# Performance work log

Measured on AMD Instinct MI355X. Metric: run time of the kernel, lower is better.

Reference implementation:

```python
import jax, jax.numpy as jnp
import numpy as np

B, N, C, H = 8, 8192, 256, 8  # batch, tokens, dim, heads


def setup_inputs() -> dict:
    key = jax.random.key(0)
    ks = jax.random.split(key, 12)
    p = lambda i, shape: jax.random.normal(ks[i], shape, jnp.float32) * 0.02
    return {
        "x0": jax.random.normal(ks[0], (B, N, C), jnp.float32),
        "x1": jax.random.normal(ks[1], (B, N, C), jnp.float32),
        # relation_judger MLP (shared by both directions)
        "fc1_w": p(2, (C, 2 * C)), "fc1_b": jnp.zeros((C,), jnp.float32),
        "fc2_w": p(3, (C, C)), "fc2_b": jnp.zeros((C,), jnp.float32),
        # cross_attn_0_to_1
        "in_w_01": p(4, (3 * C, C)), "in_b_01": jnp.zeros((3 * C,), jnp.float32),
        "out_w_01": p(5, (C, C)), "out_b_01": jnp.zeros((C,), jnp.float32),
        # cross_attn_1_to_0
        "in_w_10": p(6, (3 * C, C)), "in_b_10": jnp.zeros((3 * C,), jnp.float32),
        "out_w_10": p(7, (C, C)), "out_b_10": jnp.zeros((C,), jnp.float32),
        # noise embeddings (2 rows each)
        "k_noise": p(8, (2, C)), "v_noise": p(9, (2, C)),
    }


def _judge(a, b, fc1_w, fc1_b, fc2_w, fc2_b):
    # Mlp2(2C->C->C) + softmax over channels; torch GELU default = exact erf
    h = jax.nn.gelu(jnp.concatenate([a, b], axis=-1) @ fc1_w.T + fc1_b, approximate=False)
    return jax.nn.softmax(h @ fc2_w.T + fc2_b, axis=-1)


def _mha_kv2(q, k, v, Wi, bi, Wo, bo):
    # q: [B,N,C]; k,v: [B,N,2,C]. Each token attends over its own 2 kv slots
    # (matches torch MHA with batch_first=False, seq_q=1, seq_kv=2, batch=N).
    hd = C // H
    Q = (q @ Wi[:C].T + bi[:C]).reshape(B, N, H, hd)
    K = (k @ Wi[C:2 * C].T + bi[C:2 * C]).reshape(B, N, 2, H, hd)
    V = (v @ Wi[2 * C:].T + bi[2 * C:]).reshape(B, N, 2, H, hd)
    scores = jnp.einsum('bnhd,bnkhd->bnhk', Q, K) / jnp.sqrt(jnp.asarray(hd, q.dtype))
    attn = jax.nn.softmax(scores, axis=-1)  # [B,N,H,2]
    ctx = jnp.einsum('bnhk,bnkhd->bnhd', attn, V).reshape(B, N, C)
    return ctx @ Wo.T + bo


def reference(x0, x1, fc1_w, fc1_b, fc2_w, fc2_b,
              in_w_01, in_b_01, out_w_01, out_b_01,
              in_w_10, in_b_10, out_w_10, out_b_10,
              k_noise, v_noise):
    # noise expansion was under @torch.no_grad() -> detach noise weights
    kn = jax.lax.stop_gradient(k_noise)
    vn = jax.lax.stop_gradient(v_noise)

    rel01 = _judge(x0, x1, fc1_w, fc1_b, fc2_w, fc2_b)       # [B,N,C]
    k01 = jnp.stack([x0 + kn[0], x0 * rel01], axis=2)        # [B,N,2,C]
    v01 = jnp.stack([x0 + vn[0], x1], axis=2)
    out01 = _mha_kv2(x0, k01, v01, in_w_01, in_b_01, out_w_01, out_b_01)

    rel10 = _judge(x1, x0, fc1_w, fc1_b, fc2_w, fc2_b)
    k10 = jnp.stack([x1 + kn[1], x1 * rel10], axis=2)
    v10 = jnp.stack([x1 + vn[1], x0], axis=2)
    out10 = _mha_kv2(x1, k10, v10, in_w_10, in_b_10, out_w_10, out_b_10)

    return x0 + out01, x1 + out10
```

## Files before the change

### kernel.cpp

```cpp
#include <hip/hip_runtime.h>
#include <cstdint>
#include <cstddef>


typedef __attribute__((ext_vector_type(4))) float  f32x4;
typedef __attribute__((ext_vector_type(8))) short  short8;
typedef __attribute__((ext_vector_type(4))) float  float4_t;
typedef __attribute__((ext_vector_type(4))) unsigned short ushort4_t;

__device__ __forceinline__ float b2f(unsigned short u) {
  unsigned int x = ((unsigned int)u) << 16;
  return __builtin_bit_cast(float, x);
}
__device__ __forceinline__ unsigned short f2b(float f) {
  unsigned int u = __builtin_bit_cast(unsigned int, f);
  unsigned int r = (u + 0x7fffu + ((u >> 16) & 1u)) >> 16;
  return (unsigned short)r;
}

__device__ __forceinline__ void async16(const void* g, void* l) {
  __builtin_amdgcn_global_load_lds(
      (const __attribute__((address_space(1))) void*)g,
      (__attribute__((address_space(3))) void*)l, 16, 0, 0);
}

template <int EPI>
__global__ __launch_bounds__(256)
void gemm_bt(const unsigned short* __restrict__ A1,
             const unsigned short* __restrict__ A2,
             const unsigned short* __restrict__ W,
             int ldw, int koff2, int npairs,
             const float* __restrict__ bias,
             const float* __restrict__ res,
             void* __restrict__ outp, int ldo)
{
  __shared__ unsigned short Asm[128 * 32];
  __shared__ unsigned short Wsm[128 * 32];

  const int t = threadIdx.x;
  const size_t Arow0 = (size_t)blockIdx.x * 128;
  const int    Wrow0 = blockIdx.y * 128;

  const int l  = t & 63;
  const int wv = t >> 6;
  const int wr = (wv >> 1) * 64;
  const int wc = (wv & 1) * 64;
  const int lr = l & 15;
  const int kc = (l >> 4) * 8;

  const int srow = t >> 2;
  const int scol = (t & 3) * 8;

  f32x4 acc[4][4] = {};

  for (int p = 0; p < npairs; ++p) {
    const unsigned short* A = p ? A2 : A1;
    const int kb = p ? koff2 : 0;
    for (int kt = 0; kt < 8; ++kt) {
      const int k0 = kt * 32;
      __syncthreads();
      async16(&A[(Arow0 + srow) * 256 + (k0 + scol)],        &Asm[srow * 32 + scol]);
      async16(&A[(Arow0 + 64 + srow) * 256 + (k0 + scol)],   &Asm[(64 + srow) * 32 + scol]);
      async16(&W[(size_t)(Wrow0 + srow) * ldw + (kb + k0 + scol)],      &Wsm[srow * 32 + scol]);
      async16(&W[(size_t)(Wrow0 + 64 + srow) * ldw + (kb + k0 + scol)], &Wsm[(64 + srow) * 32 + scol]);
      __syncthreads();

      short8 af[4], bfr[4];
#pragma unroll
      for (int m = 0; m < 4; ++m)
        af[m] = *(const short8*)&Asm[(wr + m * 16 + lr) * 32 + kc];
#pragma unroll
      for (int n = 0; n < 4; ++n)
        bfr[n] = *(const short8*)&Wsm[(wc + n * 16 + lr) * 32 + kc];
#pragma unroll
      for (int m = 0; m < 4; ++m)
#pragma unroll
        for (int n = 0; n < 4; ++n)
          acc[m][n] = __builtin_amdgcn_mfma_f32_16x16x32_bf16(af[m], bfr[n], acc[m][n], 0, 0, 0);
    }
  }

  const int lq = l >> 4;
#pragma unroll
  for (int m = 0; m < 4; ++m) {
#pragma unroll
    for (int n = 0; n < 4; ++n) {
#pragma unroll
      for (int r = 0; r < 4; ++r) {
        size_t row = Arow0 + wr + m * 16 + lq * 4 + r;
        int col = Wrow0 + wc + n * 16 + lr;
        float v = acc[m][n][r] + bias[col];
        if (EPI == 1)
          v = 0.5f * v * (1.0f + erff(v * 0.70710678118654752f));
        if (EPI == 2)
          ((float*)outp)[row * (size_t)ldo + col] = v + res[row * 256 + col];
        else
          ((unsigned short*)outp)[row * (size_t)ldo + col] = f2b(v);
      }
    }
  }
}

__global__ __launch_bounds__(256)
void cvt_bf16(const float* __restrict__ src, unsigned short* __restrict__ dst, int n)
{
  int i = (blockIdx.x * 256 + threadIdx.x) * 4;
  if (i >= n) return;
  float4_t v = *(const float4_t*)(src + i);
  ushort4_t o;
  o[0] = f2b(v[0]); o[1] = f2b(v[1]); o[2] = f2b(v[2]); o[3] = f2b(v[3]);
  *(ushort4_t*)(dst + i) = o;
}

__global__ __launch_bounds__(256)
void softmax_rows(unsigned short* __restrict__ buf)
{
  int row = blockIdx.x * 4 + (threadIdx.x >> 6);
  int l = threadIdx.x & 63;
  unsigned short* p = buf + (size_t)row * 256;
  float v[4];
#pragma unroll
  for (int j = 0; j < 4; ++j) v[j] = b2f(p[l + 64 * j]);
  float mx = fmaxf(fmaxf(v[0], v[1]), fmaxf(v[2], v[3]));
#pragma unroll
  for (int off = 32; off > 0; off >>= 1) mx = fmaxf(mx, __shfl_xor(mx, off, 64));
  float s = 0.f;
#pragma unroll
  for (int j = 0; j < 4; ++j) { v[j] = expf(v[j] - mx); s += v[j]; }
#pragma unroll
  for (int off = 32; off > 0; off >>= 1) s += __shfl_xor(s, off, 64);
  float inv = 1.f / s;
#pragma unroll
  for (int j = 0; j < 4; ++j) p[l + 64 * j] = f2b(v[j] * inv);
}

__global__ __launch_bounds__(256)
void mul_bf16(const unsigned short* __restrict__ a,
              const unsigned short* __restrict__ b,
              unsigned short* __restrict__ o)
{
  size_t i = ((size_t)blockIdx.x * 256 + threadIdx.x) * 8;
  short8 va = *(const short8*)(a + i);
  short8 vb = *(const short8*)(b + i);
  short8 vo;
#pragma unroll
  for (int j = 0; j < 8; ++j)
    vo[j] = (short)f2b(b2f((unsigned short)va[j]) * b2f((unsigned short)vb[j]));
  *(short8*)(o + i) = vo;
}

__global__ __launch_bounds__(256)
void attn2(const unsigned short* __restrict__ qkv,
           const unsigned short* __restrict__ k1b,
           const unsigned short* __restrict__ v1b,
           unsigned short* __restrict__ ctx)
{
  int tid = blockIdx.x * 256 + threadIdx.x;
  int tok = tid >> 3;
  int h = tid & 7;
  const unsigned short* q   = qkv + (size_t)tok * 768 + h * 32;
  const unsigned short* k0p = q + 256;
  const unsigned short* v0p = q + 512;
  const unsigned short* k1p = k1b + (size_t)tok * 256 + h * 32;
  const unsigned short* v1p = v1b + (size_t)tok * 256 + h * 32;
  unsigned short* op = ctx + (size_t)tok * 256 + h * 32;

  float s0 = 0.f, s1 = 0.f;
#pragma unroll
  for (int c = 0; c < 4; ++c) {
    short8 q8 = *(const short8*)(q + c * 8);
    short8 a8 = *(const short8*)(k0p + c * 8);
    short8 b8 = *(const short8*)(k1p + c * 8);
#pragma unroll
    for (int j = 0; j < 8; ++j) {
      float qf = b2f((unsigned short)q8[j]);
      s0 += qf * b2f((unsigned short)a8[j]);
      s1 += qf * b2f((unsigned short)b8[j]);
    }
  }
  const float sc = 0.17677669529663687f;
  s0 *= sc; s1 *= sc;
  float mx = fmaxf(s0, s1);
  float e0 = expf(s0 - mx), e1 = expf(s1 - mx);
  float inv = 1.f / (e0 + e1);
  e0 *= inv; e1 *= inv;
#pragma unroll
  for (int c = 0; c < 4; ++c) {
    short8 a8 = *(const short8*)(v0p + c * 8);
    short8 b8 = *(const short8*)(v1p + c * 8);
    short8 o8;
#pragma unroll
    for (int j = 0; j < 8; ++j)
      o8[j] = (short)f2b(e0 * b2f((unsigned short)a8[j]) + e1 * b2f((unsigned short)b8[j]));
    *(short8*)(op + c * 8) = o8;
  }
}

__global__ __launch_bounds__(256)
void rowvec_k(const float* __restrict__ in_w, const float* __restrict__ in_b,
              const float* __restrict__ kn, const float* __restrict__ vn,
              int drow, float* __restrict__ rv)
{
  int j = blockIdx.x * 256 + threadIdx.x;
  float v = in_b[j];
  if (j >= 256) {
    const float* nz = (j < 512 ? kn : vn) + drow * 256;
    const float* wrow = in_w + (size_t)j * 256;
    float s = 0.f;
    for (int k = 0; k < 256; ++k) s += nz[k] * wrow[k];
    v += s;
  }
  rv[j] = v;
}

extern "C" void kernel_launch(void* const* d_in, const int* in_sizes, int n_in,
                              void* d_out, int out_size, void* d_ws, size_t ws_size,
                              hipStream_t stream)
{
  const float* x0     = (const float*)d_in[0];
  const float* x1     = (const float*)d_in[1];
  const float* fc1_w  = (const float*)d_in[2];
  const float* fc1_b  = (const float*)d_in[3];
  const float* fc2_w  = (const float*)d_in[4];
  const float* fc2_b  = (const float*)d_in[5];
  const float* in_w01 = (const float*)d_in[6];
  const float* in_b01 = (const float*)d_in[7];
  const float* out_w01= (const float*)d_in[8];
  const float* out_b01= (const float*)d_in[9];
  const float* in_w10 = (const float*)d_in[10];
  const float* in_b10 = (const float*)d_in[11];
  const float* out_w10= (const float*)d_in[12];
  const float* out_b10= (const float*)d_in[13];
  const float* kn     = (const float*)d_in[14];
  const float* vn     = (const float*)d_in[15];

  const size_t BN = (size_t)8 * 8192;
  const size_t NC = BN * 256;

  char* ws = (char*)d_ws;
  unsigned short* xb0   = (unsigned short*)ws; ws += NC * 2;
  unsigned short* xb1   = (unsigned short*)ws; ws += NC * 2;
  unsigned short* wfc1  = (unsigned short*)ws; ws += 131072 * 2;
  unsigned short* wfc2  = (unsigned short*)ws; ws += 65536 * 2;
  unsigned short* win01 = (unsigned short*)ws; ws += 196608 * 2;
  unsigned short* wout01= (unsigned short*)ws; ws += 65536 * 2;
  unsigned short* win10 = (unsigned short*)ws; ws += 196608 * 2;
  unsigned short* wout10= (unsigned short*)ws; ws += 65536 * 2;
  float* rv01 = (float*)ws; ws += 768 * 4;
  float* rv10 = (float*)ws; ws += 768 * 4;
  unsigned short* bufA = (unsigned short*)ws; ws += NC * 2;
  unsigned short* bufB = (unsigned short*)ws; ws += NC * 2;
  unsigned short* k1b  = (unsigned short*)ws; ws += NC * 2;
  unsigned short* v1b  = (unsigned short*)ws; ws += NC * 2;
  unsigned short* qkv  = (unsigned short*)ws; ws += BN * 768 * 2;

  size_t need = (size_t)(ws - (char*)d_ws);
  if (ws_size < need) return;

  dim3 blk(256);

  cvt_bf16<<<16384, blk, 0, stream>>>(x0, xb0, (int)NC);
  cvt_bf16<<<16384, blk, 0, stream>>>(x1, xb1, (int)NC);
  cvt_bf16<<<128, blk, 0, stream>>>(fc1_w, wfc1, 131072);
  cvt_bf16<<<64,  blk, 0, stream>>>(fc2_w, wfc2, 65536);
  cvt_bf16<<<192, blk, 0, stream>>>(in_w01, win01, 196608);
  cvt_bf16<<<64,  blk, 0, stream>>>(out_w01, wout01, 65536);
  cvt_bf16<<<192, blk, 0, stream>>>(in_w10, win10, 196608);
  cvt_bf16<<<64,  blk, 0, stream>>>(out_w10, wout10, 65536);
  rowvec_k<<<3, blk, 0, stream>>>(in_w01, in_b01, kn, vn, 0, rv01);
  rowvec_k<<<3, blk, 0, stream>>>(in_w10, in_b10, kn, vn, 1, rv10);

  for (int d = 0; d < 2; ++d) {
    const unsigned short* xa  = d ? xb1 : xb0;
    const unsigned short* xo  = d ? xb0 : xb1;
    const float* xaf  = d ? x1 : x0;
    const unsigned short* win  = d ? win10 : win01;
    const unsigned short* wout = d ? wout10 : wout01;
    const float* inb  = d ? in_b10 : in_b01;
    const float* outb = d ? out_b10 : out_b01;
    const float* rv   = d ? rv10 : rv01;
    float* outp = (float*)d_out + (size_t)d * NC;

    dim3 g2(512, 2), g6(512, 6);

    gemm_bt<1><<<g2, blk, 0, stream>>>(xa, xo, wfc1, 512, 256, 2,
                                       fc1_b, nullptr, bufA, 256);
    gemm_bt<0><<<g2, blk, 0, stream>>>(bufA, nullptr, wfc2, 256, 0, 1,
                                       fc2_b, nullptr, bufB, 256);
    softmax_rows<<<16384, blk, 0, stream>>>(bufB);
    mul_bf16<<<8192, blk, 0, stream>>>(xa, bufB, bufA);
    gemm_bt<0><<<g6, blk, 0, stream>>>(xa, nullptr, win, 256, 0, 1,
                                       rv, nullptr, qkv, 768);
    gemm_bt<0><<<g2, blk, 0, stream>>>(bufA, nullptr, win + 256 * 256, 256, 0, 1,
                                       inb + 256, nullptr, k1b, 256);
    gemm_bt<0><<<g2, blk, 0, stream>>>(xo, nullptr, win + 512 * 256, 256, 0, 1,
                                       inb + 512, nullptr, v1b, 256);
    attn2<<<2048, blk, 0, stream>>>(qkv, k1b, v1b, bufB);
    gemm_bt<2><<<g2, blk, 0, stream>>>(bufB, nullptr, wout, 256, 0, 1,
                                       outb, xaf, outp, 256);
  }
}
```

Measured before the change: 844.8 us.

## Batch both directions into merged GEMM launches with swizzled LDS and fused softmax-mul

Both attention directions are processed in single launches. One large GEMM kernel computes QKV, the cross V projection and fc1+GELU from a concatenated weight matrix, and later GEMMs cover both halves. The LDS layout is XOR-swizzled to cut bank conflicts, and workgroup IDs are remapped into chunks for cache locality. Softmax and the elementwise multiply are fused, and the conversion and prep kernels are merged. This cuts launch count and intermediate traffic, at the cost of more complex indexing and buffer aliasing (ctx reuses xb).

```diff
diff --git a/kernel.cpp b/kernel.cpp
--- a/kernel.cpp
+++ b/kernel.cpp
@@ -2,6 +2,10 @@
 #include <cstdint>
 #include <cstddef>
 
+
+#define BNv  65536
+#define TBNv 131072
+#define NCv  16777216ull
 
 typedef __attribute__((ext_vector_type(4))) float  f32x4;
 typedef __attribute__((ext_vector_type(8))) short  short8;
@@ -24,34 +28,25 @@
       (__attribute__((address_space(3))) void*)l, 16, 0, 0);
 }
 
-template <int EPI>
-__global__ __launch_bounds__(256)
-void gemm_bt(const unsigned short* __restrict__ A1,
-             const unsigned short* __restrict__ A2,
-             const unsigned short* __restrict__ W,
-             int ldw, int koff2, int npairs,
-             const float* __restrict__ bias,
-             const float* __restrict__ res,
-             void* __restrict__ outp, int ldo)
-{
-  __shared__ unsigned short Asm[128 * 32];
-  __shared__ unsigned short Wsm[128 * 32];
-
-  const int t = threadIdx.x;
-  const size_t Arow0 = (size_t)blockIdx.x * 128;
-  const int    Wrow0 = blockIdx.y * 128;
-
+__device__ __forceinline__ void mfma_loop(
+    const unsigned short* __restrict__ A1,
+    const unsigned short* __restrict__ A2,
+    const unsigned short* __restrict__ W,
+    int ldw, int koff2, int npairs,
+    size_t Arow0, int Wrow0,
+    unsigned short* Asm, unsigned short* Wsm,
+    f32x4 (&acc)[4][4], int t)
+{
   const int l  = t & 63;
   const int wv = t >> 6;
   const int wr = (wv >> 1) * 64;
   const int wc = (wv & 1) * 64;
   const int lr = l & 15;
-  const int kc = (l >> 4) * 8;
-
-  const int srow = t >> 2;
-  const int scol = (t & 3) * 8;
-
-  f32x4 acc[4][4] = {};
+  const int kcS = (((l >> 4) ^ ((lr >> 1) & 3)) * 8);
+
+  const int srow  = t >> 2;
+  const int scolS = (((t & 3) ^ ((t >> 3) & 3)) * 8);
+  const int ldst  = t * 8;
 
   for (int p = 0; p < npairs; ++p) {
     const unsigned short* A = p ? A2 : A1;
@@ -59,19 +54,19 @@
     for (int kt = 0; kt < 8; ++kt) {
       const int k0 = kt * 32;
       __syncthreads();
-      async16(&A[(Arow0 + srow) * 256 + (k0 + scol)],        &Asm[srow * 32 + scol]);
-      async16(&A[(Arow0 + 64 + srow) * 256 + (k0 + scol)],   &Asm[(64 + srow) * 32 + scol]);
-      async16(&W[(size_t)(Wrow0 + srow) * ldw + (kb + k0 + scol)],      &Wsm[srow * 32 + scol]);
-      async16(&W[(size_t)(Wrow0 + 64 + srow) * ldw + (kb + k0 + scol)], &Wsm[(64 + srow) * 32 + scol]);
+      async16(&A[(Arow0 + srow) * 256 + (size_t)(k0 + scolS)],        &Asm[ldst]);
+      async16(&A[(Arow0 + 64 + srow) * 256 + (size_t)(k0 + scolS)],   &Asm[64 * 32 + ldst]);
+      async16(&W[(size_t)(Wrow0 + srow) * ldw + (kb + k0 + scolS)],      &Wsm[ldst]);
+      async16(&W[(size_t)(Wrow0 + 64 + srow) * ldw + (kb + k0 + scolS)], &Wsm[64 * 32 + ldst]);
       __syncthreads();
 
       short8 af[4], bfr[4];
 #pragma unroll
       for (int m = 0; m < 4; ++m)
-        af[m] = *(const short8*)&Asm[(wr + m * 16 + lr) * 32 + kc];
+        af[m] = *(const short8*)&Asm[(wr + m * 16 + lr) * 32 + kcS];
 #pragma unroll
       for (int n = 0; n < 4; ++n)
-        bfr[n] = *(const short8*)&Wsm[(wc + n * 16 + lr) * 32 + kc];
+        bfr[n] = *(const short8*)&Wsm[(wc + n * 16 + lr) * 32 + kcS];
 #pragma unroll
       for (int m = 0; m < 4; ++m)
 #pragma unroll
@@ -79,31 +74,160 @@
           acc[m][n] = __builtin_amdgcn_mfma_f32_16x16x32_bf16(af[m], bfr[n], acc[m][n], 0, 0, 0);
     }
   }
-
-  const int lq = l >> 4;
+}
+
+template <int EPI>
+__device__ __forceinline__ void store_tile(
+    f32x4 (&acc)[4][4], int t,
+    const float* __restrict__ bias,
+    const float* __restrict__ res,
+    void* __restrict__ outp,
+    int ldo)
+{
+  const int l = t & 63, wv = t >> 6;
+  const int wr = (wv >> 1) * 64, wc = (wv & 1) * 64;
+  const int lr = l & 15, lq = l >> 4;
 #pragma unroll
   for (int m = 0; m < 4; ++m) {
 #pragma unroll
     for (int n = 0; n < 4; ++n) {
 #pragma unroll
       for (int r = 0; r < 4; ++r) {
-        size_t row = Arow0 + wr + m * 16 + lq * 4 + r;
-        int col = Wrow0 + wc + n * 16 + lr;
-        float v = acc[m][n][r] + bias[col];
+        int rowi = wr + m * 16 + lq * 4 + r;
+        int coli = wc + n * 16 + lr;
+        float v = acc[m][n][r] + bias[coli];
         if (EPI == 1)
           v = 0.5f * v * (1.0f + erff(v * 0.70710678118654752f));
         if (EPI == 2)
-          ((float*)outp)[row * (size_t)ldo + col] = v + res[row * 256 + col];
+          ((float*)outp)[(size_t)rowi * ldo + coli] = v + res[(size_t)rowi * 256 + coli];
         else
-          ((unsigned short*)outp)[row * (size_t)ldo + col] = f2b(v);
+          ((unsigned short*)outp)[(size_t)rowi * ldo + coli] = f2b(v);
       }
     }
   }
 }
 
 __global__ __launch_bounds__(256)
-void cvt_bf16(const float* __restrict__ src, unsigned short* __restrict__ dst, int n)
-{
+void gemm_mega(const unsigned short* __restrict__ xb,
+               const unsigned short* __restrict__ Wcat0,
+               const unsigned short* __restrict__ Wcat1,
+               const unsigned short* __restrict__ wfc1,
+               const float* __restrict__ bcat0,
+               const float* __restrict__ bcat1,
+               const float* __restrict__ fc1_b,
+               unsigned short* __restrict__ qkv,
+               unsigned short* __restrict__ v1b,
+               unsigned short* __restrict__ hbuf)
+{
+  __shared__ unsigned short Asm[128 * 32];
+  __shared__ unsigned short Wsm[128 * 32];
+  const int t = threadIdx.x;
+
+  const int nwg = 10240, BPC = 160;
+  int bid  = blockIdx.x;
+  int wgid = (bid & 7) * (nwg >> 3) + (bid >> 3);
+  int chunk = wgid / BPC, rem = wgid % BPC;
+  int x = chunk * 16 + rem / 10;
+  int y = rem % 10;
+
+  const int half = x >> 9;
+  const size_t tok0 = (size_t)(x & 511) * 128;
+  const unsigned short* A1 = xb + (size_t)half * (BNv * 256);
+
+  f32x4 acc[4][4] = {};
+
+  if (y < 8) {
+    const unsigned short* W = half ? Wcat1 : Wcat0;
+    const float* bias = (half ? bcat1 : bcat0) + y * 128;
+    mfma_loop(A1, nullptr, W, 256, 0, 1, tok0, y * 128, Asm, Wsm, acc, t);
+    if (y < 6) {
+      size_t row0 = (size_t)half * BNv + tok0;
+      store_tile<0>(acc, t, bias, nullptr, qkv + row0 * 768 + y * 128, 768);
+    } else {
+      size_t row0 = (size_t)(1 - half) * BNv + tok0;
+      store_tile<0>(acc, t, bias, nullptr, v1b + row0 * 256 + (y - 6) * 128, 256);
+    }
+  } else {
+    const unsigned short* A2 = xb + (size_t)(1 - half) * (BNv * 256);
+    mfma_loop(A1, A2, wfc1, 512, 256, 2, tok0, (y - 8) * 128, Asm, Wsm, acc, t);
+    size_t row0 = (size_t)half * BNv + tok0;
+    store_tile<1>(acc, t, fc1_b + (y - 8) * 128, nullptr,
+                  hbuf + row0 * 256 + (y - 8) * 128, 256);
+  }
+}
+
+template <int EPI>
+__global__ __launch_bounds__(256)
+void gemm_b2(const unsigned short* __restrict__ A,
+             const unsigned short* __restrict__ W0,
+             const unsigned short* __restrict__ W1,
+             const float* __restrict__ b0, const float* __restrict__ b1,
+             const float* __restrict__ res0, const float* __restrict__ res1,
+             void* __restrict__ outp)
+{
+  __shared__ unsigned short Asm[128 * 32];
+  __shared__ unsigned short Wsm[128 * 32];
+  const int t = threadIdx.x;
+
+  const int nwg = 2048;
+  int bid  = blockIdx.x;
+  int wgid = (bid & 7) * (nwg >> 3) + (bid >> 3);
+  int chunk = wgid >> 5, rem = wgid & 31;
+  int x = chunk * 16 + (rem >> 1);
+  int y = rem & 1;
+
+  const int half = x >> 9;
+  const size_t row0 = (size_t)x * 128;
+
+  f32x4 acc[4][4] = {};
+  mfma_loop(A, nullptr, half ? W1 : W0, 256, 0, 1, row0, y * 128, Asm, Wsm, acc, t);
+
+  const float* bias = (half ? b1 : b0) + y * 128;
+  if (EPI == 2) {
+    const float* res = (half ? res1 : res0) + (row0 - (size_t)half * BNv) * 256 + y * 128;
+    store_tile<2>(acc, t, bias, res, (float*)outp + row0 * 256 + y * 128, 256);
+  } else {
+    store_tile<0>(acc, t, bias, nullptr,
+                  (unsigned short*)outp + row0 * 256 + y * 128, 256);
+  }
+}
+
+
+__global__ __launch_bounds__(256)
+void cvt_x(const float* __restrict__ x0, const float* __restrict__ x1,
+           unsigned short* __restrict__ xb)
+{
+  size_t i = ((size_t)blockIdx.x * 256 + threadIdx.x) * 8;
+  const float* s = (i < NCv) ? (x0 + i) : (x1 + (i - NCv));
+  float4_t a = *(const float4_t*)s;
+  float4_t b = *(const float4_t*)(s + 4);
+  short8 o;
+  o[0] = (short)f2b(a[0]); o[1] = (short)f2b(a[1]);
+  o[2] = (short)f2b(a[2]); o[3] = (short)f2b(a[3]);
+  o[4] = (short)f2b(b[0]); o[5] = (short)f2b(b[1]);
+  o[6] = (short)f2b(b[2]); o[7] = (short)f2b(b[3]);
+  *(short8*)(xb + i) = o;
+}
+
+__global__ __launch_bounds__(256)
+void prep_w(const float* fc1_w, const float* fc2_w,
+            const float* in_w01, const float* out_w01,
+            const float* in_w10, const float* out_w10,
+            unsigned short* wfc1, unsigned short* wfc2,
+            unsigned short* Wcat0, unsigned short* Wcat1,
+            unsigned short* wout0, unsigned short* wout1)
+{
+  const float* src; unsigned short* dst; int n;
+  switch (blockIdx.y) {
+    case 0: src = fc1_w;             dst = wfc1;             n = 131072; break;
+    case 1: src = fc2_w;             dst = wfc2;             n = 65536;  break;
+    case 2: src = in_w01;            dst = Wcat0;            n = 196608; break;
+    case 3: src = in_w10 + 512*256;  dst = Wcat0 + 768*256;  n = 65536;  break;
+    case 4: src = in_w10;            dst = Wcat1;            n = 196608; break;
+    case 5: src = in_w01 + 512*256;  dst = Wcat1 + 768*256;  n = 65536;  break;
+    case 6: src = out_w01;           dst = wout0;            n = 65536;  break;
+    default: src = out_w10;          dst = wout1;            n = 65536;  break;
+  }
   int i = (blockIdx.x * 256 + threadIdx.x) * 4;
   if (i >= n) return;
   float4_t v = *(const float4_t*)(src + i);
@@ -113,40 +237,53 @@
 }
 
 __global__ __launch_bounds__(256)
-void softmax_rows(unsigned short* __restrict__ buf)
-{
-  int row = blockIdx.x * 4 + (threadIdx.x >> 6);
+void prep_bcat(const float* in_w01, const float* in_b01,
+               const float* in_w10, const float* in_b10,
+               const float* kn, const float* vn,
+               float* bcat0, float* bcat1)
+{
+  int j = blockIdx.x * 256 + threadIdx.x;
+  int h = j >> 10, c = j & 1023;
+  const float* inw  = h ? in_w10 : in_w01;
+  const float* inb  = h ? in_b10 : in_b01;
+  const float* oinb = h ? in_b01 : in_b10;
+  float v;
+  if (c < 256) v = inb[c];
+  else if (c < 768) {
+    const float* nz = (c < 512 ? kn : vn) + h * 256;
+    const float* wrow = inw + (size_t)c * 256;
+    float s = 0.f;
+    for (int k = 0; k < 256; ++k) s += nz[k] * wrow[k];
+    v = inb[c] + s;
+  } else v = oinb[512 + (c - 768)];
+  (h ? bcat1 : bcat0)[c] = v;
+}
+
+__global__ __launch_bounds__(256)
+void softmax_mul(const unsigned short* __restrict__ s,
+                 const unsigned short* __restrict__ xb,
+                 unsigned short* __restrict__ k1in)
+{
+  size_t row = (size_t)blockIdx.x * 4 + (threadIdx.x >> 6);
   int l = threadIdx.x & 63;
-  unsigned short* p = buf + (size_t)row * 256;
+  const unsigned short* p = s + row * 256;
   float v[4];
 #pragma unroll
   for (int j = 0; j < 4; ++j) v[j] = b2f(p[l + 64 * j]);
   float mx = fmaxf(fmaxf(v[0], v[1]), fmaxf(v[2], v[3]));
 #pragma unroll
   for (int off = 32; off > 0; off >>= 1) mx = fmaxf(mx, __shfl_xor(mx, off, 64));
-  float s = 0.f;
-#pragma unroll
-  for (int j = 0; j < 4; ++j) { v[j] = expf(v[j] - mx); s += v[j]; }
-#pragma unroll
-  for (int off = 32; off > 0; off >>= 1) s += __shfl_xor(s, off, 64);
-  float inv = 1.f / s;
-#pragma unroll
-  for (int j = 0; j < 4; ++j) p[l + 64 * j] = f2b(v[j] * inv);
-}
-
-__global__ __launch_bounds__(256)
-void mul_bf16(const unsigned short* __restrict__ a,
-              const unsigned short* __restrict__ b,
-              unsigned short* __restrict__ o)
-{
-  size_t i = ((size_t)blockIdx.x * 256 + threadIdx.x) * 8;
-  short8 va = *(const short8*)(a + i);
-  short8 vb = *(const short8*)(b + i);
-  short8 vo;
-#pragma unroll
-  for (int j = 0; j < 8; ++j)
-    vo[j] = (short)f2b(b2f((unsigned short)va[j]) * b2f((unsigned short)vb[j]));
-  *(short8*)(o + i) = vo;
+  float sum = 0.f;
+#pragma unroll
+  for (int j = 0; j < 4; ++j) { v[j] = expf(v[j] - mx); sum += v[j]; }
+#pragma unroll
+  for (int off = 32; off > 0; off >>= 1) sum += __shfl_xor(sum, off, 64);
+  float inv = 1.f / sum;
+  const unsigned short* xr = xb + row * 256;
+  unsigned short* o = k1in + row * 256;
+#pragma unroll
+  for (int j = 0; j < 4; ++j)
+    o[l + 64 * j] = f2b(v[j] * inv * b2f(xr[l + 64 * j]));
 }
 
 __global__ __launch_bounds__(256)
@@ -156,14 +293,14 @@
            unsigned short* __restrict__ ctx)
 {
   int tid = blockIdx.x * 256 + threadIdx.x;
-  int tok = tid >> 3;
+  size_t tok = (size_t)(tid >> 3);
   int h = tid & 7;
-  const unsigned short* q   = qkv + (size_t)tok * 768 + h * 32;
+  const unsigned short* q   = qkv + tok * 768 + h * 32;
   const unsigned short* k0p = q + 256;
   const unsigned short* v0p = q + 512;
-  const unsigned short* k1p = k1b + (size_t)tok * 256 + h * 32;
-  const unsigned short* v1p = v1b + (size_t)tok * 256 + h * 32;
-  unsigned short* op = ctx + (size_t)tok * 256 + h * 32;
+  const unsigned short* k1p = k1b + tok * 256 + h * 32;
+  const unsigned short* v1p = v1b + tok * 256 + h * 32;
+  unsigned short* op = ctx + tok * 256 + h * 32;
 
   float s0 = 0.f, s1 = 0.f;
 #pragma unroll
@@ -194,23 +331,6 @@
       o8[j] = (short)f2b(e0 * b2f((unsigned short)a8[j]) + e1 * b2f((unsigned short)b8[j]));
     *(short8*)(op + c * 8) = o8;
   }
-}
-
-__global__ __launch_bounds__(256)
-void rowvec_k(const float* __restrict__ in_w, const float* __restrict__ in_b,
-              const float* __restrict__ kn, const float* __restrict__ vn,
-              int drow, float* __restrict__ rv)
-{
-  int j = blockIdx.x * 256 + threadIdx.x;
-  float v = in_b[j];
-  if (j >= 256) {
-    const float* nz = (j < 512 ? kn : vn) + drow * 256;
-    const float* wrow = in_w + (size_t)j * 256;
-    float s = 0.f;
-    for (int k = 0; k < 256; ++k) s += nz[k] * wrow[k];
-    v += s;
-  }
-  rv[j] = v;
 }
 
 extern "C" void kernel_launch(void* const* d_in, const int* in_sizes, int n_in,
@@ -234,69 +354,44 @@
   const float* kn     = (const float*)d_in[14];
   const float* vn     = (const float*)d_in[15];
 
-  const size_t BN = (size_t)8 * 8192;
-  const size_t NC = BN * 256;
-
   char* ws = (char*)d_ws;
-  unsigned short* xb0   = (unsigned short*)ws; ws += NC * 2;
-  unsigned short* xb1   = (unsigned short*)ws; ws += NC * 2;
-  unsigned short* wfc1  = (unsigned short*)ws; ws += 131072 * 2;
-  unsigned short* wfc2  = (unsigned short*)ws; ws += 65536 * 2;
-  unsigned short* win01 = (unsigned short*)ws; ws += 196608 * 2;
-  unsigned short* wout01= (unsigned short*)ws; ws += 65536 * 2;
-  unsigned short* win10 = (unsigned short*)ws; ws += 196608 * 2;
-  unsigned short* wout10= (unsigned short*)ws; ws += 65536 * 2;
-  float* rv01 = (float*)ws; ws += 768 * 4;
-  float* rv10 = (float*)ws; ws += 768 * 4;
-  unsigned short* bufA = (unsigned short*)ws; ws += NC * 2;
-  unsigned short* bufB = (unsigned short*)ws; ws += NC * 2;
-  unsigned short* k1b  = (unsigned short*)ws; ws += NC * 2;
-  unsigned short* v1b  = (unsigned short*)ws; ws += NC * 2;
-  unsigned short* qkv  = (unsigned short*)ws; ws += BN * 768 * 2;
-
-  size_t need = (size_t)(ws - (char*)d_ws);
-  if (ws_size < need) return;
+  unsigned short* xb   = (unsigned short*)ws; ws += TBNv * 256 * 2;
+  unsigned short* qkv  = (unsigned short*)ws; ws += (size_t)TBNv * 768 * 2;
+  unsigned short* v1b  = (unsigned short*)ws; ws += TBNv * 256 * 2;
+  unsigned short* hbuf = (unsigned short*)ws; ws += TBNv * 256 * 2;
+  unsigned short* sbuf = (unsigned short*)ws; ws += TBNv * 256 * 2;
+  unsigned short* wfc1 = (unsigned short*)ws; ws += 131072 * 2;
+  unsigned short* wfc2 = (unsigned short*)ws; ws += 65536 * 2;
+  unsigned short* Wcat0= (unsigned short*)ws; ws += 262144 * 2;
+  unsigned short* Wcat1= (unsigned short*)ws; ws += 262144 * 2;
+  unsigned short* wout0= (unsigned short*)ws; ws += 65536 * 2;
+  unsigned short* wout1= (unsigned short*)ws; ws += 65536 * 2;
+  float* bcat0 = (float*)ws; ws += 1024 * 4;
+  float* bcat1 = (float*)ws; ws += 1024 * 4;
+
+  unsigned short* k1in = hbuf;
+  unsigned short* k1b  = sbuf;
+  unsigned short* ctx  = xb;
+
+  if (ws_size < (size_t)(ws - (char*)d_ws)) return;
 
   dim3 blk(256);
 
-  cvt_bf16<<<16384, blk, 0, stream>>>(x0, xb0, (int)NC);
-  cvt_bf16<<<16384, blk, 0, stream>>>(x1, xb1, (int)NC);
-  cvt_bf16<<<128, blk, 0, stream>>>(fc1_w, wfc1, 131072);
-  cvt_bf16<<<64,  blk, 0, stream>>>(fc2_w, wfc2, 65536);
-  cvt_bf16<<<192, blk, 0, stream>>>(in_w01, win01, 196608);
-  cvt_bf16<<<64,  blk, 0, stream>>>(out_w01, wout01, 65536);
-  cvt_bf16<<<192, blk, 0, stream>>>(in_w10, win10, 196608);
-  cvt_bf16<<<64,  blk, 0, stream>>>(out_w10, wout10, 65536);
-  rowvec_k<<<3, blk, 0, stream>>>(in_w01, in_b01, kn, vn, 0, rv01);
-  rowvec_k<<<3, blk, 0, stream>>>(in_w10, in_b10, kn, vn, 1, rv10);
-
-  for (int d = 0; d < 2; ++d) {
-    const unsigned short* xa  = d ? xb1 : xb0;
-    const unsigned short* xo  = d ? xb0 : xb1;
-    const float* xaf  = d ? x1 : x0;
-    const unsigned short* win  = d ? win10 : win01;
-    const unsigned short* wout = d ? wout10 : wout01;
-    const float* inb  = d ? in_b10 : in_b01;
-    const float* outb = d ? out_b10 : out_b01;
-    const float* rv   = d ? rv10 : rv01;
-    float* outp = (float*)d_out + (size_t)d * NC;
-
-    dim3 g2(512, 2), g6(512, 6);
-
-    gemm_bt<1><<<g2, blk, 0, stream>>>(xa, xo, wfc1, 512, 256, 2,
-                                       fc1_b, nullptr, bufA, 256);
-    gemm_bt<0><<<g2, blk, 0, stream>>>(bufA, nullptr, wfc2, 256, 0, 1,
-                                       fc2_b, nullptr, bufB, 256);
-    softmax_rows<<<16384, blk, 0, stream>>>(bufB);
-    mul_bf16<<<8192, blk, 0, stream>>>(xa, bufB, bufA);
-    gemm_bt<0><<<g6, blk, 0, stream>>>(xa, nullptr, win, 256, 0, 1,
-                                       rv, nullptr, qkv, 768);
-    gemm_bt<0><<<g2, blk, 0, stream>>>(bufA, nullptr, win + 256 * 256, 256, 0, 1,
-                                       inb + 256, nullptr, k1b, 256);
-    gemm_bt<0><<<g2, blk, 0, stream>>>(xo, nullptr, win + 512 * 256, 256, 0, 1,
-                                       inb + 512, nullptr, v1b, 256);
-    attn2<<<2048, blk, 0, stream>>>(qkv, k1b, v1b, bufB);
-    gemm_bt<2><<<g2, blk, 0, stream>>>(bufB, nullptr, wout, 256, 0, 1,
-                                       outb, xaf, outp, 256);
-  }
-}
+  cvt_x<<<16384, blk, 0, stream>>>(x0, x1, xb);
+  prep_w<<<dim3(192, 8), blk, 0, stream>>>(fc1_w, fc2_w, in_w01, out_w01,
+                                           in_w10, out_w10,
+                                           wfc1, wfc2, Wcat0, Wcat1, wout0, wout1);
+  prep_bcat<<<8, blk, 0, stream>>>(in_w01, in_b01, in_w10, in_b10, kn, vn,
+                                   bcat0, bcat1);
+  gemm_mega<<<10240, blk, 0, stream>>>(xb, Wcat0, Wcat1, wfc1,
+                                       bcat0, bcat1, fc1_b, qkv, v1b, hbuf);
+  gemm_b2<0><<<2048, blk, 0, stream>>>(hbuf, wfc2, wfc2, fc2_b, fc2_b,
+                                       nullptr, nullptr, sbuf);
+  softmax_mul<<<32768, blk, 0, stream>>>(sbuf, xb, k1in);
+  gemm_b2<0><<<2048, blk, 0, stream>>>(k1in, Wcat0 + 256 * 256, Wcat1 + 256 * 256,
+                                       in_b01 + 256, in_b10 + 256,
+                                       nullptr, nullptr, k1b);
+  attn2<<<4096, blk, 0, stream>>>(qkv, k1b, v1b, ctx);
+  gemm_b2<2><<<2048, blk, 0, stream>>>(ctx, wout0, wout1, out_b01, out_b10,
+                                       x0, x1, d_out);
+}
```

New measurement: 751.8 us. -11.0%, faster.
